# Kernel optimization log

Hardware: AMD Instinct MI355X
Metric: run time of the kernel (lower is better)

Reference implementation:

```python
import jax, jax.numpy as jnp
import numpy as np

ALPHA = 0.15
KSIZE = 5
EPS = 1e-6


def _minmax_norm(x):
    # x: [B,1,H,W]; per-sample min-max normalize, 0.5 if nearly constant
    mn = x.min(axis=(1, 2, 3), keepdims=True)
    mx = x.max(axis=(1, 2, 3), keepdims=True)
    denom = mx - mn
    safe = jnp.where(denom > EPS, denom, 1.0)
    return jnp.where(denom > EPS, (x - mn) / safe, 0.5)


def _saliency_map(images, out_hw):
    # grayscale via luma weights
    w = jnp.array([0.299, 0.587, 0.114], dtype=images.dtype).reshape(1, 3, 1, 1)
    gray = (images * w).sum(axis=1, keepdims=True)  # [B,1,H,W]
    kernel = jnp.ones((1, 1, KSIZE, KSIZE), dtype=gray.dtype) / (KSIZE * KSIZE)
    dn = ('NCHW', 'OIHW', 'NCHW')
    local_mean = jax.lax.conv_general_dilated(gray, kernel, (1, 1), 'SAME', dimension_numbers=dn)
    local_mean_sq = jax.lax.conv_general_dilated(gray ** 2, kernel, (1, 1), 'SAME', dimension_numbers=dn)
    local_var = jnp.maximum(local_mean_sq - local_mean ** 2, 0.0)
    sal = _minmax_norm(local_var)
    if sal.shape[-2:] != out_hw:
        sal = jax.image.resize(sal, (sal.shape[0], 1, out_hw[0], out_hw[1]), method='bilinear')
    return jax.lax.stop_gradient(sal)  # computed under no_grad / detached in torch


def setup_inputs() -> dict:
    key = jax.random.key(0)
    k1, k2 = jax.random.split(key)
    features = jax.random.normal(k1, (64, 512, 28, 28), dtype=jnp.float32)
    images = jax.random.uniform(k2, (64, 3, 224, 224), dtype=jnp.float32)
    return {"features": features, "images": images}


def reference(features, images):
    sal = _saliency_map(images, features.shape[-2:])  # [B,1,Hf,Wf]
    attn = jnp.sqrt((features ** 2).mean(axis=1, keepdims=True))  # [B,1,Hf,Wf]
    attn = _minmax_norm(attn)
    loss = jnp.mean((attn - sal) ** 2)
    return ALPHA * loss
```

## Files before the change

### kernel.cpp

```cpp
#include <hip/hip_runtime.h>
#include <math.h>

#define BATCH 64
#define HIMG 224
#define WIMG 224
#define IMGPLANE (HIMG*WIMG)
#define CF 512
#define HF 28
#define WF 28
#define POS (HF*WF)
#define ALPHA_C 0.15f
#define EPS_C 1e-6f

#define STRIPS 14
#define SROWS 16
#define GROWS 20
#define GSTR 229
#define VSTR 261
#define SHN 4580

#define ZG 16
#define ZCH 32

#define OFF_HRES 0
#define HRES_CNT (BATCH*HIMG*WF)
#define OFF_BMM (OFF_HRES + HRES_CNT)
#define OFF_AP  (OFF_BMM + BATCH*STRIPS*2)
#define OFF_ACC (OFF_AP + ZG*BATCH*POS)
#define OFF_CNT (OFF_ACC + 1)

__global__ __launch_bounds__(256) void attn_k(const float* __restrict__ f,
                                              float* __restrict__ ws) {
    int z = blockIdx.x, b = blockIdx.y;
    int tid = threadIdx.x;
    if (z == 0 && b == 0 && tid == 0) {
        ws[OFF_ACC] = 0.0f;
        ((unsigned*)ws)[OFF_CNT] = 0u;
    }
    if (tid >= 196) return;
    const float* fp = f + (size_t)(b * CF + z * ZCH) * POS + 4 * tid;
    float ax = 0.0f, ay = 0.0f, az = 0.0f, aw = 0.0f;
    #pragma unroll
    for (int c = 0; c < ZCH; c++) {
        float4 u = *(const float4*)(fp + (size_t)c * POS);
        ax += u.x * u.x; ay += u.y * u.y;
        az += u.z * u.z; aw += u.w * u.w;
    }
    *(float4*)(ws + OFF_AP + (size_t)(z * BATCH + b) * POS + 4 * tid) =
        make_float4(ax, ay, az, aw);
}

__global__ __launch_bounds__(256) void varh_k(const float* __restrict__ img,
                                              float* __restrict__ ws) {
    __shared__ float sh[SHN];
    __shared__ float wred[8];
    int sy = blockIdx.x, b = blockIdx.y;
    int tid = threadIdx.x;
    int y0 = sy * SROWS;
    const float* imb = img + (size_t)b * 3 * IMGPLANE;

    for (int i = tid; i < GROWS * 56; i += 256) {
        int gr = i / 56, q = i - gr * 56;
        int gy = y0 - 2 + gr;
        float gx0 = 0.0f, gx1 = 0.0f, gx2 = 0.0f, gx3 = 0.0f;
        if ((unsigned)gy < HIMG) {
            const float* row = imb + gy * WIMG + 4 * q;
            float4 a = *(const float4*)(row);
            float4 bb = *(const float4*)(row + IMGPLANE);
            float4 c = *(const float4*)(row + 2 * IMGPLANE);
            gx0 = 0.299f * a.x + 0.587f * bb.x + 0.114f * c.x;
            gx1 = 0.299f * a.y + 0.587f * bb.y + 0.114f * c.y;
            gx2 = 0.299f * a.z + 0.587f * bb.z + 0.114f * c.z;
            gx3 = 0.299f * a.w + 0.587f * bb.w + 0.114f * c.w;
        }
        int base = gr * GSTR + 2 + 4 * q;
        sh[base] = gx0; sh[base + 1] = gx1; sh[base + 2] = gx2; sh[base + 3] = gx3;
    }
    if (tid < GROWS * 4) {
        int gr = tid >> 2, p = tid & 3;
        int gc = (p < 2) ? p : (224 + p);
        sh[gr * GSTR + gc] = 0.0f;
    }
    __syncthreads();

    int r = tid >> 4, s = tid & 15;
    int x0 = 14 * s;
    const float* gr0 = sh + r * GSTR;
    float c1[5], c2[5], vreg[14];
    #pragma unroll
    for (int m = 0; m < 5; m++) {
        float a = 0.0f, a2 = 0.0f;
        #pragma unroll
        for (int k = 0; k < 5; k++) {
            float u = gr0[k * GSTR + x0 + m];
            a += u; a2 += u * u;
        }
        c1[m] = a; c2[m] = a2;
    }
    float vmn = INFINITY, vmx = 0.0f;
    #pragma unroll
    for (int xi = 0; xi < 14; xi++) {
        int p = xi % 5;
        float s1 = c1[p], s2 = c2[p];
        #pragma unroll
        for (int m = 1; m < 5; m++) {
            s1 += c1[(p + m) % 5];
            s2 += c2[(p + m) % 5];
        }
        float m1 = s1 * 0.04f, m2 = s2 * 0.04f;
        float vv = fmaxf(m2 - m1 * m1, 0.0f);
        vreg[xi] = vv;
        vmn = fminf(vmn, vv); vmx = fmaxf(vmx, vv);
        if (xi < 13) {
            float a = 0.0f, a2 = 0.0f;
            #pragma unroll
            for (int k = 0; k < 5; k++) {
                float u = gr0[k * GSTR + x0 + xi + 5];
                a += u; a2 += u * u;
            }
            c1[p] = a; c2[p] = a2;
        }
    }
    #pragma unroll
    for (int o = 32; o > 0; o >>= 1) {
        vmn = fminf(vmn, __shfl_xor(vmn, o));
        vmx = fmaxf(vmx, __shfl_xor(vmx, o));
    }
    __syncthreads();
    int w = tid >> 6;
    if ((tid & 63) == 0) { wred[w] = vmn; wred[4 + w] = vmx; }
    if (tid < SROWS * 8) {
        int rr = tid >> 3, p = tid & 7;
        int jh = p + ((p < 4) ? 0 : 224);
        sh[rr * VSTR + jh + (jh >> 3)] = 0.0f;
    }
    #pragma unroll
    for (int xi = 0; xi < 14; xi++) {
        int jh = x0 + xi + 4;
        sh[r * VSTR + jh + (jh >> 3)] = vreg[xi];
    }
    __syncthreads();
    if (tid == 0) {
        float mn = fminf(fminf(wred[0], wred[1]), fminf(wred[2], wred[3]));
        float mx = fmaxf(fmaxf(wred[4], wred[5]), fmaxf(wred[6], wred[7]));
        int blk = b * STRIPS + sy;
        ws[OFF_BMM + 2 * blk]     = mn;
        ws[OFF_BMM + 2 * blk + 1] = mx;
    }

    float* hb = ws + OFF_HRES + ((size_t)b * HIMG + y0) * WF;
    for (int idx = tid; idx < SROWS * WF; idx += 256) {
        int rr = idx / WF, i = idx - rr * WF;
        float acc = 0.0f, wsum = 0.0f;
        int j0 = 8 * i - 4;
        #pragma unroll
        for (int t = 0; t < 16; t++) {
            int j = j0 + t;
            float w_ = 8.0f - fabsf((float)t - 7.5f);
            int jh = j + 4;
            acc += w_ * sh[rr * VSTR + jh + (jh >> 3)];
            if ((unsigned)j < WIMG) wsum += w_;
        }
        hb[idx] = acc / wsum;
    }
}

__global__ __launch_bounds__(256) void fused_k(float* __restrict__ ws,
                                               float* __restrict__ out) {
    __shared__ float hres[HIMG][WF + 1];
    __shared__ float wred[4];
    __shared__ float s_mn, s_mx;
    int b = blockIdx.x;
    int tid = threadIdx.x;

    if (tid < 64) {
        float mn = INFINITY, mx = 0.0f;
        if (tid < STRIPS) {
            mn = ws[OFF_BMM + 2 * (b * STRIPS + tid)];
            mx = ws[OFF_BMM + 2 * (b * STRIPS + tid) + 1];
        }
        #pragma unroll
        for (int o = 8; o > 0; o >>= 1) {
            mn = fminf(mn, __shfl_down(mn, o));
            mx = fmaxf(mx, __shfl_down(mx, o));
        }
        if (tid == 0) { s_mn = mn; s_mx = mx; }
    }

    const float* hg = ws + OFF_HRES + (size_t)b * HIMG * WF;
    for (int i = tid; i < HIMG * WF; i += 256) {
        int y = i / WF, x = i - y * WF;
        hres[y][x] = hg[i];
    }
    __syncthreads();

    float vmn = s_mn, vmx = s_mx;
    float vden = vmx - vmn;
    bool vok = vden > EPS_C;

    const float* ap = ws + OFF_AP + (size_t)b * POS;
    float salv[4], attnv[4];
    float amn = INFINITY, amx = -INFINITY;
    #pragma unroll
    for (int k = 0; k < 4; k++) {
        int idx = tid + 256 * k;
        salv[k] = 0.0f; attnv[k] = 0.0f;
        if (idx < POS) {
            int yo = idx / WF, x = idx - yo * WF;
            float acc = 0.0f, wsum = 0.0f;
            int j0 = 8 * yo - 4;
            #pragma unroll
            for (int t = 0; t < 16; t++) {
                int j = j0 + t;
                float w = 8.0f - fabsf((float)t - 7.5f);
                if ((unsigned)j < HIMG) { acc += w * hres[j][x]; wsum += w; }
            }
            float sraw = acc / wsum;
            salv[k] = vok ? (sraw - vmn) / vden : 0.5f;
            float ssum = 0.0f;
            #pragma unroll
            for (int z = 0; z < ZG; z++)
                ssum += ap[(size_t)z * BATCH * POS + idx];
            float a = sqrtf(ssum * (1.0f / CF));
            attnv[k] = a;
            amn = fminf(amn, a); amx = fmaxf(amx, a);
        }
    }

    #pragma unroll
    for (int o = 32; o > 0; o >>= 1) {
        amn = fminf(amn, __shfl_xor(amn, o));
        amx = fmaxf(amx, __shfl_xor(amx, o));
    }
    int w = tid >> 6;
    if ((tid & 63) == 0) wred[w] = amn;
    __syncthreads();
    if (tid == 0) s_mn = fminf(fminf(wred[0], wred[1]), fminf(wred[2], wred[3]));
    __syncthreads();
    if ((tid & 63) == 0) wred[w] = amx;
    __syncthreads();
    if (tid == 0) s_mx = fmaxf(fmaxf(wred[0], wred[1]), fmaxf(wred[2], wred[3]));
    __syncthreads();
    amn = s_mn; amx = s_mx;
    float aden = amx - amn;
    bool aok = aden > EPS_C;

    float lsum = 0.0f;
    #pragma unroll
    for (int k = 0; k < 4; k++) {
        int idx = tid + 256 * k;
        if (idx < POS) {
            float an = aok ? (attnv[k] - amn) / aden : 0.5f;
            float d = an - salv[k];
            lsum += d * d;
        }
    }
    #pragma unroll
    for (int o = 32; o > 0; o >>= 1) lsum += __shfl_xor(lsum, o);
    if ((tid & 63) == 0) wred[w] = lsum;
    __syncthreads();

    if (tid == 0) {
        float part = wred[0] + wred[1] + wred[2] + wred[3];
        atomicAdd(ws + OFF_ACC, part);
        __threadfence();
        unsigned old = atomicAdd((unsigned*)ws + OFF_CNT, 1u);
        if (old == BATCH - 1) {
            float tot = atomicAdd(ws + OFF_ACC, 0.0f);
            out[0] = tot * (ALPHA_C / (float)(BATCH * POS));
        }
    }
}

extern "C" void kernel_launch(void* const* d_in, const int* in_sizes, int n_in,
                              void* d_out, int out_size, void* d_ws, size_t ws_size,
                              hipStream_t stream) {
    const float* features = (const float*)d_in[0];
    const float* images   = (const float*)d_in[1];
    float* ws  = (float*)d_ws;
    float* out = (float*)d_out;

    hipLaunchKernelGGL(attn_k,  dim3(ZG, BATCH),     dim3(256), 0, stream, features, ws);
    hipLaunchKernelGGL(varh_k,  dim3(STRIPS, BATCH), dim3(256), 0, stream, images, ws);
    hipLaunchKernelGGL(fused_k, dim3(BATCH),         dim3(256), 0, stream, ws, out);
}
```

Before: 193.9 us.

## Merge attention, variance and finalize kernels into one kernel with per-batch last-block finalize

Replaces the three-kernel pipeline with a tiny init kernel plus one combined kernel. Its blocks are split per batch between feature-channel reduction and image-strip variance work, and the last block to finish for each batch (detected via a per-batch atomic counter) performs the resize, normalization and loss. This removes inter-kernel launch gaps and lets the feature and image work run concurrently. The trade-off is a larger shared-memory footprint for every block and serialized finalize work in the tail blocks. The attention loop also now uses two accumulator sets to expose more independent loads.

```diff
diff --git a/kernel.cpp b/kernel.cpp
--- a/kernel.cpp
+++ b/kernel.cpp
@@ -17,161 +17,175 @@
 #define GROWS 20
 #define GSTR 229
 #define VSTR 261
-#define SHN 4580
 
 #define ZG 16
 #define ZCH 32
+#define NBPS (ZG + STRIPS)
+
+#define SHW 29
+#define SHN 6528
 
 #define OFF_HRES 0
 #define HRES_CNT (BATCH*HIMG*WF)
 #define OFF_BMM (OFF_HRES + HRES_CNT)
 #define OFF_AP  (OFF_BMM + BATCH*STRIPS*2)
-#define OFF_ACC (OFF_AP + ZG*BATCH*POS)
+#define OFF_CNTS (OFF_AP + ZG*BATCH*POS)
+#define OFF_ACC (OFF_CNTS + BATCH)
 #define OFF_CNT (OFF_ACC + 1)
 
-__global__ __launch_bounds__(256) void attn_k(const float* __restrict__ f,
-                                              float* __restrict__ ws) {
-    int z = blockIdx.x, b = blockIdx.y;
-    int tid = threadIdx.x;
-    if (z == 0 && b == 0 && tid == 0) {
-        ws[OFF_ACC] = 0.0f;
-        ((unsigned*)ws)[OFF_CNT] = 0u;
-    }
-    if (tid >= 196) return;
-    const float* fp = f + (size_t)(b * CF + z * ZCH) * POS + 4 * tid;
-    float ax = 0.0f, ay = 0.0f, az = 0.0f, aw = 0.0f;
-    #pragma unroll
-    for (int c = 0; c < ZCH; c++) {
-        float4 u = *(const float4*)(fp + (size_t)c * POS);
-        ax += u.x * u.x; ay += u.y * u.y;
-        az += u.z * u.z; aw += u.w * u.w;
-    }
-    *(float4*)(ws + OFF_AP + (size_t)(z * BATCH + b) * POS + 4 * tid) =
-        make_float4(ax, ay, az, aw);
+__global__ void init_k(float* ws) {
+    int t = threadIdx.x;
+    if (t < BATCH) ((unsigned*)ws)[OFF_CNTS + t] = 0u;
+    if (t == BATCH) ws[OFF_ACC] = 0.0f;
+    if (t == BATCH + 1) ((unsigned*)ws)[OFF_CNT] = 0u;
 }
 
-__global__ __launch_bounds__(256) void varh_k(const float* __restrict__ img,
-                                              float* __restrict__ ws) {
+__global__ __launch_bounds__(256) void mega_k(const float* __restrict__ img,
+                                              const float* __restrict__ f,
+                                              float* __restrict__ ws,
+                                              float* __restrict__ out) {
     __shared__ float sh[SHN];
     __shared__ float wred[8];
-    int sy = blockIdx.x, b = blockIdx.y;
-    int tid = threadIdx.x;
-    int y0 = sy * SROWS;
-    const float* imb = img + (size_t)b * 3 * IMGPLANE;
-
-    for (int i = tid; i < GROWS * 56; i += 256) {
-        int gr = i / 56, q = i - gr * 56;
-        int gy = y0 - 2 + gr;
-        float gx0 = 0.0f, gx1 = 0.0f, gx2 = 0.0f, gx3 = 0.0f;
-        if ((unsigned)gy < HIMG) {
-            const float* row = imb + gy * WIMG + 4 * q;
-            float4 a = *(const float4*)(row);
-            float4 bb = *(const float4*)(row + IMGPLANE);
-            float4 c = *(const float4*)(row + 2 * IMGPLANE);
-            gx0 = 0.299f * a.x + 0.587f * bb.x + 0.114f * c.x;
-            gx1 = 0.299f * a.y + 0.587f * bb.y + 0.114f * c.y;
-            gx2 = 0.299f * a.z + 0.587f * bb.z + 0.114f * c.z;
-            gx3 = 0.299f * a.w + 0.587f * bb.w + 0.114f * c.w;
-        }
-        int base = gr * GSTR + 2 + 4 * q;
-        sh[base] = gx0; sh[base + 1] = gx1; sh[base + 2] = gx2; sh[base + 3] = gx3;
-    }
-    if (tid < GROWS * 4) {
-        int gr = tid >> 2, p = tid & 3;
-        int gc = (p < 2) ? p : (224 + p);
-        sh[gr * GSTR + gc] = 0.0f;
-    }
-    __syncthreads();
-
-    int r = tid >> 4, s = tid & 15;
-    int x0 = 14 * s;
-    const float* gr0 = sh + r * GSTR;
-    float c1[5], c2[5], vreg[14];
-    #pragma unroll
-    for (int m = 0; m < 5; m++) {
-        float a = 0.0f, a2 = 0.0f;
-        #pragma unroll
-        for (int k = 0; k < 5; k++) {
-            float u = gr0[k * GSTR + x0 + m];
-            a += u; a2 += u * u;
-        }
-        c1[m] = a; c2[m] = a2;
-    }
-    float vmn = INFINITY, vmx = 0.0f;
-    #pragma unroll
-    for (int xi = 0; xi < 14; xi++) {
-        int p = xi % 5;
-        float s1 = c1[p], s2 = c2[p];
-        #pragma unroll
-        for (int m = 1; m < 5; m++) {
-            s1 += c1[(p + m) % 5];
-            s2 += c2[(p + m) % 5];
-        }
-        float m1 = s1 * 0.04f, m2 = s2 * 0.04f;
-        float vv = fmaxf(m2 - m1 * m1, 0.0f);
-        vreg[xi] = vv;
-        vmn = fminf(vmn, vv); vmx = fmaxf(vmx, vv);
-        if (xi < 13) {
-            float a = 0.0f, a2 = 0.0f;
+    __shared__ float s_mn, s_mx;
+    __shared__ int s_last;
+    int bid = blockIdx.x, tid = threadIdx.x;
+    int b = bid / NBPS, r = bid - NBPS * b;
+
+    if (r < ZG) {
+        int z = r;
+        if (tid < 196) {
+            const float* fp = f + (size_t)(b * CF + z * ZCH) * POS + 4 * tid;
+            float ax = 0, ay = 0, az = 0, aw = 0;
+            float bx = 0, by = 0, bz = 0, bw = 0;
+            #pragma unroll
+            for (int c = 0; c < ZCH; c += 2) {
+                float4 u = *(const float4*)(fp + (size_t)c * POS);
+                float4 v = *(const float4*)(fp + (size_t)(c + 1) * POS);
+                ax += u.x * u.x; ay += u.y * u.y; az += u.z * u.z; aw += u.w * u.w;
+                bx += v.x * v.x; by += v.y * v.y; bz += v.z * v.z; bw += v.w * v.w;
+            }
+            *(float4*)(ws + OFF_AP + (size_t)(z * BATCH + b) * POS + 4 * tid) =
+                make_float4(ax + bx, ay + by, az + bz, aw + bw);
+        }
+    } else {
+        int sy = r - ZG;
+        int y0 = sy * SROWS;
+        const float* imb = img + (size_t)b * 3 * IMGPLANE;
+
+        for (int i = tid; i < GROWS * 56; i += 256) {
+            int gr = i / 56, q = i - gr * 56;
+            int gy = y0 - 2 + gr;
+            float g0 = 0, g1 = 0, g2 = 0, g3 = 0;
+            if ((unsigned)gy < HIMG) {
+                const float* row = imb + gy * WIMG + 4 * q;
+                float4 a = *(const float4*)(row);
+                float4 bb = *(const float4*)(row + IMGPLANE);
+                float4 c = *(const float4*)(row + 2 * IMGPLANE);
+                g0 = 0.299f * a.x + 0.587f * bb.x + 0.114f * c.x;
+                g1 = 0.299f * a.y + 0.587f * bb.y + 0.114f * c.y;
+                g2 = 0.299f * a.z + 0.587f * bb.z + 0.114f * c.z;
+                g3 = 0.299f * a.w + 0.587f * bb.w + 0.114f * c.w;
+            }
+            int base = gr * GSTR + 2 + 4 * q;
+            sh[base] = g0; sh[base + 1] = g1; sh[base + 2] = g2; sh[base + 3] = g3;
+        }
+        if (tid < GROWS * 4) {
+            int gr = tid >> 2, p = tid & 3;
+            int gc = (p < 2) ? p : (224 + p);
+            sh[gr * GSTR + gc] = 0.0f;
+        }
+        __syncthreads();
+
+        int rr = tid >> 4, s = tid & 15;
+        int x0 = 14 * s;
+        const float* gr0 = sh + rr * GSTR;
+        float c1[5], c2[5], vreg[14];
+        #pragma unroll
+        for (int m = 0; m < 5; m++) {
+            float a = 0, a2 = 0;
             #pragma unroll
             for (int k = 0; k < 5; k++) {
-                float u = gr0[k * GSTR + x0 + xi + 5];
+                float u = gr0[k * GSTR + x0 + m];
                 a += u; a2 += u * u;
             }
-            c1[p] = a; c2[p] = a2;
-        }
-    }
-    #pragma unroll
-    for (int o = 32; o > 0; o >>= 1) {
-        vmn = fminf(vmn, __shfl_xor(vmn, o));
-        vmx = fmaxf(vmx, __shfl_xor(vmx, o));
-    }
-    __syncthreads();
-    int w = tid >> 6;
-    if ((tid & 63) == 0) { wred[w] = vmn; wred[4 + w] = vmx; }
-    if (tid < SROWS * 8) {
-        int rr = tid >> 3, p = tid & 7;
-        int jh = p + ((p < 4) ? 0 : 224);
-        sh[rr * VSTR + jh + (jh >> 3)] = 0.0f;
-    }
-    #pragma unroll
-    for (int xi = 0; xi < 14; xi++) {
-        int jh = x0 + xi + 4;
-        sh[r * VSTR + jh + (jh >> 3)] = vreg[xi];
-    }
+            c1[m] = a; c2[m] = a2;
+        }
+        float vmn = INFINITY, vmx = 0.0f;
+        #pragma unroll
+        for (int xi = 0; xi < 14; xi++) {
+            int p = xi % 5;
+            float s1 = c1[p], s2 = c2[p];
+            #pragma unroll
+            for (int m = 1; m < 5; m++) {
+                s1 += c1[(p + m) % 5];
+                s2 += c2[(p + m) % 5];
+            }
+            float m1 = s1 * 0.04f, m2 = s2 * 0.04f;
+            float vv = fmaxf(m2 - m1 * m1, 0.0f);
+            vreg[xi] = vv;
+            vmn = fminf(vmn, vv); vmx = fmaxf(vmx, vv);
+            if (xi < 13) {
+                float a = 0, a2 = 0;
+                #pragma unroll
+                for (int k = 0; k < 5; k++) {
+                    float u = gr0[k * GSTR + x0 + xi + 5];
+                    a += u; a2 += u * u;
+                }
+                c1[p] = a; c2[p] = a2;
+            }
+        }
+        #pragma unroll
+        for (int o = 32; o > 0; o >>= 1) {
+            vmn = fminf(vmn, __shfl_xor(vmn, o));
+            vmx = fmaxf(vmx, __shfl_xor(vmx, o));
+        }
+        __syncthreads();
+        int w = tid >> 6;
+        if ((tid & 63) == 0) { wred[w] = vmn; wred[4 + w] = vmx; }
+        if (tid < SROWS * 8) {
+            int r2 = tid >> 3, p = tid & 7;
+            int jh = p + ((p < 4) ? 0 : 224);
+            sh[r2 * VSTR + jh + (jh >> 3)] = 0.0f;
+        }
+        #pragma unroll
+        for (int xi = 0; xi < 14; xi++) {
+            int jh = x0 + xi + 4;
+            sh[rr * VSTR + jh + (jh >> 3)] = vreg[xi];
+        }
+        __syncthreads();
+        if (tid == 0) {
+            float mn = fminf(fminf(wred[0], wred[1]), fminf(wred[2], wred[3]));
+            float mx = fmaxf(fmaxf(wred[4], wred[5]), fmaxf(wred[6], wred[7]));
+            int blk = b * STRIPS + sy;
+            ws[OFF_BMM + 2 * blk]     = mn;
+            ws[OFF_BMM + 2 * blk + 1] = mx;
+        }
+        float* hb = ws + OFF_HRES + ((size_t)b * HIMG + y0) * WF;
+        for (int idx = tid; idx < SROWS * WF; idx += 256) {
+            int r3 = idx / WF, i = idx - r3 * WF;
+            float acc = 0.0f, wsum = 0.0f;
+            int j0 = 8 * i - 4;
+            #pragma unroll
+            for (int t = 0; t < 16; t++) {
+                int j = j0 + t;
+                float w_ = 8.0f - fabsf((float)t - 7.5f);
+                int jh = j + 4;
+                acc += w_ * sh[r3 * VSTR + jh + (jh >> 3)];
+                if ((unsigned)j < WIMG) wsum += w_;
+            }
+            hb[idx] = acc / wsum;
+        }
+    }
+
     __syncthreads();
     if (tid == 0) {
-        float mn = fminf(fminf(wred[0], wred[1]), fminf(wred[2], wred[3]));
-        float mx = fmaxf(fmaxf(wred[4], wred[5]), fmaxf(wred[6], wred[7]));
-        int blk = b * STRIPS + sy;
-        ws[OFF_BMM + 2 * blk]     = mn;
-        ws[OFF_BMM + 2 * blk + 1] = mx;
-    }
-
-    float* hb = ws + OFF_HRES + ((size_t)b * HIMG + y0) * WF;
-    for (int idx = tid; idx < SROWS * WF; idx += 256) {
-        int rr = idx / WF, i = idx - rr * WF;
-        float acc = 0.0f, wsum = 0.0f;
-        int j0 = 8 * i - 4;
-        #pragma unroll
-        for (int t = 0; t < 16; t++) {
-            int j = j0 + t;
-            float w_ = 8.0f - fabsf((float)t - 7.5f);
-            int jh = j + 4;
-            acc += w_ * sh[rr * VSTR + jh + (jh >> 3)];
-            if ((unsigned)j < WIMG) wsum += w_;
-        }
-        hb[idx] = acc / wsum;
-    }
-}
-
-__global__ __launch_bounds__(256) void fused_k(float* __restrict__ ws,
-                                               float* __restrict__ out) {
-    __shared__ float hres[HIMG][WF + 1];
-    __shared__ float wred[4];
-    __shared__ float s_mn, s_mx;
-    int b = blockIdx.x;
-    int tid = threadIdx.x;
+        __threadfence();
+        unsigned old = atomicAdd((unsigned*)ws + OFF_CNTS + b, 1u);
+        s_last = (old == NBPS - 1) ? 1 : 0;
+    }
+    __syncthreads();
+    if (!s_last) return;
+    __threadfence();
 
     if (tid < 64) {
         float mn = INFINITY, mx = 0.0f;
@@ -186,11 +200,10 @@
         }
         if (tid == 0) { s_mn = mn; s_mx = mx; }
     }
-
     const float* hg = ws + OFF_HRES + (size_t)b * HIMG * WF;
     for (int i = tid; i < HIMG * WF; i += 256) {
         int y = i / WF, x = i - y * WF;
-        hres[y][x] = hg[i];
+        sh[y * SHW + x] = hg[i];
     }
     __syncthreads();
 
@@ -213,7 +226,7 @@
             for (int t = 0; t < 16; t++) {
                 int j = j0 + t;
                 float w = 8.0f - fabsf((float)t - 7.5f);
-                if ((unsigned)j < HIMG) { acc += w * hres[j][x]; wsum += w; }
+                if ((unsigned)j < HIMG) { acc += w * sh[j * SHW + x]; wsum += w; }
             }
             float sraw = acc / wsum;
             salv[k] = vok ? (sraw - vmn) / vden : 0.5f;
@@ -280,7 +293,7 @@
     float* ws  = (float*)d_ws;
     float* out = (float*)d_out;
 
-    hipLaunchKernelGGL(attn_k,  dim3(ZG, BATCH),     dim3(256), 0, stream, features, ws);
-    hipLaunchKernelGGL(varh_k,  dim3(STRIPS, BATCH), dim3(256), 0, stream, images, ws);
-    hipLaunchKernelGGL(fused_k, dim3(BATCH),         dim3(256), 0, stream, ws, out);
+    hipLaunchKernelGGL(init_k, dim3(1),             dim3(256), 0, stream, ws);
+    hipLaunchKernelGGL(mega_k, dim3(BATCH * NBPS),  dim3(256), 0, stream,
+                       images, features, ws, out);
 }
```

Measured after the change: 301.8 us. 1.56x slower.
